# Optimization experiments

Measured on AMD Instinct MI355X. Metric: run time of the kernel, lower is better.

## Reference

```python
import jax, jax.numpy as jnp
import numpy as np

B, H, W, C = 4, 64, 64, 512
CR = C // 8  # reduced channel dim for query/key (conv_b, conv_c)


def setup_inputs() -> dict:
    key = jax.random.key(0)
    k1, k2, k3, k4, k5 = jax.random.split(key, 5)
    x = jax.random.normal(k1, (B, H, W, C), dtype=jnp.float32)
    # 1x1 conv kernels (no bias) == dense weights applied per pixel
    Wb = jax.random.normal(k2, (C, CR), dtype=jnp.float32) * (2.0 / C) ** 0.5
    Wc = jax.random.normal(k3, (C, CR), dtype=jnp.float32) * (2.0 / C) ** 0.5
    Wd = jax.random.normal(k4, (C, C), dtype=jnp.float32) * (2.0 / C) ** 0.5
    gamma = jax.random.normal(k5, (1,), dtype=jnp.float32)
    return {"x": x, "Wb": Wb, "Wc": Wc, "Wd": Wd, "gamma": gamma}


def reference(x, Wb, Wc, Wd, gamma):
    b, h, w, c = x.shape
    n = h * w
    xf = x.reshape(b, n, c)                       # [B,N,C] flatten spatial
    q = jnp.einsum('bnc,cd->bnd', xf, Wb)         # conv_b: [B,N,CR]
    k = jnp.einsum('bnc,cd->bnd', xf, Wc)         # conv_c: [B,N,CR]
    v = jnp.einsum('bnc,cd->bnd', xf, Wd)         # conv_d: [B,N,C]
    scores = jnp.einsum('bnd,bmd->bnm', q, k)     # [B,N,N] position affinities
    attn = jax.nn.softmax(scores, axis=-1)
    out = jnp.einsum('bnm,bmc->bnc', attn, v)     # [B,N,C]
    out = out.reshape(b, h, w, c)
    return gamma * out + x
```

## Files before the change

### kernel.cpp

```cpp
#include <hip/hip_runtime.h>


typedef __bf16 bf16_t;
typedef __bf16 bf16x8 __attribute__((ext_vector_type(8)));
typedef float f32x4 __attribute__((ext_vector_type(4)));
typedef unsigned long long u64;

#define NN 4096
#define CC 512
#define VSTRIDE 4160u
#define PSTRIDE 4160u
#define ESHIFT 90.0f

#define OFF_QH 0u
#define OFF_QL 1048576u
#define OFF_KH 2097152u
#define OFF_KL 3145728u
#define OFF_VT 4194304u
#define OFF_WBH 29491200u
#define OFF_WBL 29523968u
#define OFF_WCH 29556736u
#define OFF_WCL 29589504u
#define OFF_WD  29622272u
#define OFF_XHF 46137344u
#define OFF_XLF 54525952u
#define OFF_P   12713984u
#define PBATCH  17039360u

static __device__ __forceinline__ f32x4 mfma16(bf16x8 a, bf16x8 b, f32x4 c) {
    return __builtin_amdgcn_mfma_f32_16x16x32_bf16(a, b, c, 0, 0, 0);
}

static __device__ __forceinline__ void load_lds16(const bf16_t* g, bf16_t* l) {
    __builtin_amdgcn_global_load_lds(
        (const __attribute__((address_space(1))) unsigned int*)g,
        (__attribute__((address_space(3))) unsigned int*)l, 16, 0, 0);
}

__global__ __launch_bounds__(256) void prep_kernel(const float* __restrict__ Wb,
                                                   const float* __restrict__ Wc,
                                                   const float* __restrict__ Wd,
                                                   bf16_t* __restrict__ ws) {
    int j = blockIdx.x * 256 + threadIdx.x;
    if (j < 8192) {
        const float* W = (j < 4096) ? Wb : Wc;
        unsigned oh = (j < 4096) ? OFF_WBH : OFF_WCH;
        unsigned ol = (j < 4096) ? OFF_WBL : OFF_WCL;
        int jc = j & 4095;
        int nt = jc >> 10, ks = (jc >> 6) & 15, lane = jc & 63;
        int quad = lane >> 4, l16 = lane & 15;
        int col = nt * 16 + l16, k0 = ks * 32 + quad * 8;
        bf16x8 h, l;
#pragma unroll
        for (int i = 0; i < 8; ++i) {
            float v = W[(k0 + i) * 64 + col];
            bf16_t hv = (bf16_t)v;
            h[i] = hv;
            l[i] = (bf16_t)(v - (float)hv);
        }
        *(bf16x8*)(ws + oh + (size_t)jc * 8) = h;
        *(bf16x8*)(ws + ol + (size_t)jc * 8) = l;
    } else if (j < 40960) {
        int jc = j - 8192;
        int nT = jc >> 12, nt = (jc >> 10) & 3, ks = (jc >> 6) & 15, lane = jc & 63;
        int quad = lane >> 4, l16 = lane & 15;
        int col = nT * 64 + nt * 16 + l16, k0 = ks * 32 + quad * 8;
        bf16x8 h;
#pragma unroll
        for (int i = 0; i < 8; ++i)
            h[i] = (bf16_t)Wd[(k0 + i) * 512 + col];
        *(bf16x8*)(ws + OFF_WD + (size_t)jc * 8) = h;
    }
}

__global__ __launch_bounds__(256) void xprep_kernel(const float* __restrict__ x,
                                                    bf16_t* __restrict__ ws) {
    int mt = blockIdx.x;
    int tid = threadIdx.x;
    const float* xb = x + (size_t)mt * 32768;
#pragma unroll
    for (int it = 0; it < 16; ++it) {
        int c = it * 256 + tid;
        int row = c >> 6, col8 = c & 63;
        f32x4 a0 = *(const f32x4*)(xb + c * 8);
        f32x4 a1 = *(const f32x4*)(xb + c * 8 + 4);
        bf16x8 h, l;
#pragma unroll
        for (int jj = 0; jj < 4; ++jj) {
            bf16_t h0 = (bf16_t)a0[jj];
            bf16_t h1 = (bf16_t)a1[jj];
            h[jj] = h0;     l[jj] = (bf16_t)(a0[jj] - (float)h0);
            h[4 + jj] = h1; l[4 + jj] = (bf16_t)(a1[jj] - (float)h1);
        }
        int w = row >> 4, l16 = row & 15, ks = col8 >> 2, quad = col8 & 3;
        size_t dst = (size_t)mt * 32768 + w * 8192 + ks * 512 + (quad * 16 + l16) * 8;
        *(bf16x8*)(ws + OFF_XHF + dst) = h;
        *(bf16x8*)(ws + OFF_XLF + dst) = l;
    }
}

__global__ __launch_bounds__(256, 1) void qkv_kernel(bf16_t* __restrict__ ws) {
    int mt = blockIdx.x;
    int g  = blockIdx.y;
    int tid = threadIdx.x;
    int w = tid >> 6, lane = tid & 63, quad = lane >> 4, l16 = lane & 15;

    __shared__ __align__(16) bf16_t Vs[64][72];

    size_t xoff = (size_t)mt * 32768 + w * 8192 + lane * 8;

    if (g < 2) {
        bf16x8 xh[16], xl[16];
#pragma unroll
        for (int ks = 0; ks < 16; ++ks)
            xh[ks] = *(const bf16x8*)(ws + OFF_XHF + xoff + ks * 512);
#pragma unroll
        for (int ks = 0; ks < 16; ++ks)
            xl[ks] = *(const bf16x8*)(ws + OFF_XLF + xoff + ks * 512);

        const bf16_t* whf = ws + (g == 0 ? OFF_WBH : OFF_WCH) + lane * 8;
        const bf16_t* wlf = ws + (g == 0 ? OFF_WBL : OFF_WCL) + lane * 8;
        f32x4 acc[4];
#pragma unroll
        for (int nt = 0; nt < 4; ++nt) acc[nt] = (f32x4){0.f, 0.f, 0.f, 0.f};
#pragma unroll
        for (int ks = 0; ks < 16; ++ks) {
#pragma unroll
            for (int nt = 0; nt < 4; ++nt) {
                bf16x8 bh = *(const bf16x8*)(whf + (nt * 16 + ks) * 512);
                bf16x8 bl = *(const bf16x8*)(wlf + (nt * 16 + ks) * 512);
                acc[nt] = mfma16(xh[ks], bh, acc[nt]);
                acc[nt] = mfma16(xh[ks], bl, acc[nt]);
                acc[nt] = mfma16(xl[ks], bh, acc[nt]);
            }
        }
        unsigned base_h = (g == 0) ? OFF_QH : OFF_KH;
        unsigned base_l = (g == 0) ? OFF_QL : OFF_KL;
#pragma unroll
        for (int nt = 0; nt < 4; ++nt) {
            int gc = nt * 16 + l16;
#pragma unroll
            for (int r = 0; r < 4; ++r) {
                int gr = mt * 64 + w * 16 + quad * 4 + r;
                int b = gr >> 12, np = gr & 4095;
                float v = acc[nt][r];
                bf16_t h = (bf16_t)v;
                size_t o = ((size_t)(b * 4096 + np)) * 64 + gc;
                ws[base_h + o] = h;
                ws[base_l + o] = (bf16_t)(v - (float)h);
            }
        }
    } else {
        bf16x8 xh[16];
#pragma unroll
        for (int ks = 0; ks < 16; ++ks)
            xh[ks] = *(const bf16x8*)(ws + OFF_XHF + xoff + ks * 512);

        for (int t = 0; t < 2; ++t) {
            int nT = (g - 2) * 2 + t;
            const bf16_t* wdf = ws + OFF_WD + lane * 8;
            f32x4 acc[4];
#pragma unroll
            for (int nt = 0; nt < 4; ++nt) acc[nt] = (f32x4){0.f, 0.f, 0.f, 0.f};
#pragma unroll
            for (int ks = 0; ks < 16; ++ks) {
#pragma unroll
                for (int nt = 0; nt < 4; ++nt) {
                    bf16x8 bb = *(const bf16x8*)(wdf + (size_t)(((nT * 4 + nt) * 16 + ks)) * 512);
                    acc[nt] = mfma16(xh[ks], bb, acc[nt]);
                }
            }
#pragma unroll
            for (int nt = 0; nt < 4; ++nt) {
                bf16_t pk[4];
#pragma unroll
                for (int r = 0; r < 4; ++r) pk[r] = (bf16_t)acc[nt][r];
                *(u64*)&Vs[nt * 16 + l16][w * 16 + quad * 4] = *(u64*)pk;
            }
            __syncthreads();
            int gr0 = mt * 64;
            int bb = gr0 >> 12, np0 = gr0 & 4095;
            int ch = tid >> 2, seg = tid & 3;
            f32x4 d0 = *(const f32x4*)&Vs[ch][seg * 16];
            f32x4 d1 = *(const f32x4*)&Vs[ch][seg * 16 + 8];
            bf16_t* dst = ws + OFF_VT +
                ((size_t)bb * 512 + (size_t)(nT * 64 + ch)) * VSTRIDE + np0 + seg * 16;
            *(f32x4*)(dst) = d0;
            *(f32x4*)(dst + 8) = d1;
            __syncthreads();
        }
    }
}

__global__ __launch_bounds__(256, 2) void score_kernel(bf16_t* __restrict__ ws) {
    int idx = blockIdx.x;
    int mt = idx & 31;
    int nt = (idx >> 5) & 31;
    int b  = idx >> 10;
    int tid = threadIdx.x;
    int w = tid >> 6, lane = tid & 63, quad = lane >> 4, l16 = lane & 15;
    int wr = w >> 1, wc = w & 1;

    __shared__ __align__(16) bf16_t Ls[128][136];

    const bf16_t* Qh = ws + OFF_QH + (size_t)b * NN * 64;
    const bf16_t* Ql = ws + OFF_QL + (size_t)b * NN * 64;
    const bf16_t* Kh = ws + OFF_KH + (size_t)b * NN * 64;
    const bf16_t* Kl = ws + OFF_KL + (size_t)b * NN * 64;

    bf16x8 qh[4][2], ql[4][2];
#pragma unroll
    for (int rt = 0; rt < 4; ++rt) {
        size_t qo = (size_t)(nt * 128 + wr * 64 + rt * 16 + l16) * 64 + quad * 8;
        qh[rt][0] = *(const bf16x8*)(Qh + qo);
        qh[rt][1] = *(const bf16x8*)(Qh + qo + 32);
        ql[rt][0] = *(const bf16x8*)(Ql + qo);
        ql[rt][1] = *(const bf16x8*)(Ql + qo + 32);
    }

    f32x4 s[4][4];
#pragma unroll
    for (int ct = 0; ct < 4; ++ct) {
        size_t ko = (size_t)(mt * 128 + wc * 64 + ct * 16 + l16) * 64 + quad * 8;
        bf16x8 kh0 = *(const bf16x8*)(Kh + ko);
        bf16x8 kh1 = *(const bf16x8*)(Kh + ko + 32);
        bf16x8 kl0 = *(const bf16x8*)(Kl + ko);
        bf16x8 kl1 = *(const bf16x8*)(Kl + ko + 32);
#pragma unroll
        for (int rt = 0; rt < 4; ++rt) {
            f32x4 a = (f32x4){0.f, 0.f, 0.f, 0.f};
            a = mfma16(qh[rt][0], kh0, a);
            a = mfma16(qh[rt][1], kh1, a);
            a = mfma16(qh[rt][0], kl0, a);
            a = mfma16(qh[rt][1], kl1, a);
            a = mfma16(ql[rt][0], kh0, a);
            a = mfma16(ql[rt][1], kh1, a);
            s[rt][ct] = a;
        }
    }

#pragma unroll
    for (int rt = 0; rt < 4; ++rt)
#pragma unroll
        for (int ct = 0; ct < 4; ++ct)
#pragma unroll
            for (int r = 0; r < 4; ++r) {
                float p = __expf(s[rt][ct][r] - ESHIFT);
                Ls[wr * 64 + rt * 16 + quad * 4 + r][wc * 64 + ct * 16 + l16] = (bf16_t)p;
            }
    __syncthreads();

    bf16_t* P = ws + OFF_P + (size_t)b * PBATCH;
    int row0 = tid >> 4, chunk = tid & 15;
#pragma unroll
    for (int it = 0; it < 8; ++it) {
        int row = it * 16 + row0;
        f32x4 d = *(const f32x4*)&Ls[row][chunk * 8];
        *(f32x4*)(P + (size_t)(nt * 128 + row) * PSTRIDE + mt * 128 + chunk * 8) = d;
    }
}

__global__ __launch_bounds__(256, 2) void pv_kernel(const float* __restrict__ x,
                                                    const float* __restrict__ gamma_p,
                                                    const bf16_t* __restrict__ ws,
                                                    float* __restrict__ out) {
    int idx = blockIdx.x;
    int ct4 = idx & 3;
    int b   = (idx >> 2) & 3;
    int nt  = idx >> 4;
    int tid = threadIdx.x;
    int w = tid >> 6, lane = tid & 63, quad = lane >> 4, l16 = lane & 15;
    int wr = w >> 1, wc = w & 1;

    __shared__ __align__(16) bf16_t Pt[2][4096];
    __shared__ __align__(16) bf16_t Vt[2][4096];

    const bf16_t* P = ws + OFF_P + (size_t)b * PBATCH + (size_t)(nt * 128) * PSTRIDE;
    const bf16_t* V = ws + OFF_VT + (size_t)b * CC * VSTRIDE + (size_t)(ct4 * 128) * VSTRIDE;

    int sr = tid >> 2;
    int sc = (tid & 3) ^ ((sr >> 1) & 3);
    const bf16_t* gp = P + (size_t)sr * PSTRIDE + sc * 8;
    const bf16_t* gv = V + (size_t)sr * VSTRIDE + sc * 8;

    f32x4 o[4][4];
#pragma unroll
    for (int rt = 0; rt < 4; ++rt)
#pragma unroll
        for (int ct = 0; ct < 4; ++ct) o[rt][ct] = (f32x4){0.f, 0.f, 0.f, 0.f};
    f32x4 osum[4];
#pragma unroll
    for (int rt = 0; rt < 4; ++rt) osum[rt] = (f32x4){0.f, 0.f, 0.f, 0.f};

    bf16_t onev = (bf16_t)1.0f;
    bf16x8 vones = {onev, onev, onev, onev, onev, onev, onev, onev};

    auto stage = [&](int buf, int t) {
        int m0 = t * 32;
        load_lds16(gp + m0,                  &Pt[buf][tid * 8]);
        load_lds16(gp + 64u * PSTRIDE + m0,  &Pt[buf][2048 + tid * 8]);
        load_lds16(gv + m0,                  &Vt[buf][tid * 8]);
        load_lds16(gv + 64u * VSTRIDE + m0,  &Vt[buf][2048 + tid * 8]);
    };

    auto compute = [&](int buf) {
        bf16x8 pa[4], vb[4];
#pragma unroll
        for (int rt = 0; rt < 4; ++rt) {
            int R = wr * 64 + rt * 16 + l16;
            int mc = quad ^ ((R >> 1) & 3);
            pa[rt] = *(const bf16x8*)&Pt[buf][R * 32 + mc * 8];
        }
#pragma unroll
        for (int ct = 0; ct < 4; ++ct) {
            int Rv = wc * 64 + ct * 16 + l16;
            int mc = quad ^ ((Rv >> 1) & 3);
            vb[ct] = *(const bf16x8*)&Vt[buf][Rv * 32 + mc * 8];
        }
#pragma unroll
        for (int ct = 0; ct < 4; ++ct)
#pragma unroll
            for (int rt = 0; rt < 4; ++rt)
                o[rt][ct] = mfma16(pa[rt], vb[ct], o[rt][ct]);
        if (wc == 0) {
            osum[0] = mfma16(pa[0], vones, osum[0]);
            osum[1] = mfma16(pa[1], vones, osum[1]);
            osum[2] = mfma16(pa[2], vones, osum[2]);
            osum[3] = mfma16(pa[3], vones, osum[3]);
        }
    };

    stage(0, 0);
    __syncthreads();
    for (int t = 0; t < 127; ++t) {
        int cur = t & 1;
        stage(cur ^ 1, t + 1);
        compute(cur);
        __syncthreads();
    }
    compute(1);

    float* rsum_s = (float*)&Pt[0][0];
    if (wc == 0 && l16 == 0) {
#pragma unroll
        for (int rt = 0; rt < 4; ++rt)
#pragma unroll
            for (int r = 0; r < 4; ++r)
                rsum_s[wr * 64 + rt * 16 + quad * 4 + r] = osum[rt][r];
    }
    __syncthreads();

    float g = gamma_p[0];
#pragma unroll
    for (int rt = 0; rt < 4; ++rt) {
        f32x4 rs = *(const f32x4*)&rsum_s[wr * 64 + rt * 16 + quad * 4];
        f32x4 linv;
#pragma unroll
        for (int r = 0; r < 4; ++r) linv[r] = 1.0f / rs[r];
#pragma unroll
        for (int ct = 0; ct < 4; ++ct) {
#pragma unroll
            for (int r = 0; r < 4; ++r) {
                int n = nt * 128 + wr * 64 + rt * 16 + quad * 4 + r;
                int c = ct4 * 128 + wc * 64 + ct * 16 + l16;
                size_t off = ((size_t)(b * 4096 + n)) * 512 + c;
                out[off] = g * (o[rt][ct][r] * linv[r]) + x[off];
            }
        }
    }
}

extern "C" void kernel_launch(void* const* d_in, const int* in_sizes, int n_in,
                              void* d_out, int out_size, void* d_ws, size_t ws_size,
                              hipStream_t stream) {
    const float* x     = (const float*)d_in[0];
    const float* Wb    = (const float*)d_in[1];
    const float* Wc    = (const float*)d_in[2];
    const float* Wd    = (const float*)d_in[3];
    const float* gamma = (const float*)d_in[4];
    bf16_t* ws = (bf16_t*)d_ws;
    float* out = (float*)d_out;

    prep_kernel<<<160, 256, 0, stream>>>(Wb, Wc, Wd, ws);
    xprep_kernel<<<256, 256, 0, stream>>>(x, ws);
    qkv_kernel<<<dim3(256, 6), 256, 0, stream>>>(ws);
    score_kernel<<<4096, 256, 0, stream>>>(ws);
    pv_kernel<<<512, 256, 0, stream>>>(x, gamma, ws, out);
}
```

Baseline: 322.3 us.

## Triple-buffer PV kernel LDS staging with partial vmcnt waits

Changes the P·V kernel from double to triple buffering of the P and V tiles in shared memory, keeping two tile loads in flight ahead of compute. The single __syncthreads per step becomes a partial vmcnt wait plus a barrier, so the next tile's global-to-LDS loads can stay outstanding while the current tile computes. It raises LDS use from 32KB to 48KB per block, which may limit occupancy with launch bounds of 2 blocks per CU. It also depends on vmcnt counting being exact for the buffer loads.

```diff
diff --git a/kernel.cpp b/kernel.cpp
--- a/kernel.cpp
+++ b/kernel.cpp
@@ -272,8 +272,8 @@
     int w = tid >> 6, lane = tid & 63, quad = lane >> 4, l16 = lane & 15;
     int wr = w >> 1, wc = w & 1;
 
-    __shared__ __align__(16) bf16_t Pt[2][4096];
-    __shared__ __align__(16) bf16_t Vt[2][4096];
+    __shared__ __align__(16) bf16_t PtA[3 * 4096];
+    __shared__ __align__(16) bf16_t VtA[3 * 4096];
 
     const bf16_t* P = ws + OFF_P + (size_t)b * PBATCH + (size_t)(nt * 128) * PSTRIDE;
     const bf16_t* V = ws + OFF_VT + (size_t)b * CC * VSTRIDE + (size_t)(ct4 * 128) * VSTRIDE;
@@ -297,25 +297,29 @@
 
     auto stage = [&](int buf, int t) {
         int m0 = t * 32;
-        load_lds16(gp + m0,                  &Pt[buf][tid * 8]);
-        load_lds16(gp + 64u * PSTRIDE + m0,  &Pt[buf][2048 + tid * 8]);
-        load_lds16(gv + m0,                  &Vt[buf][tid * 8]);
-        load_lds16(gv + 64u * VSTRIDE + m0,  &Vt[buf][2048 + tid * 8]);
+        bf16_t* pd = PtA + buf * 4096;
+        bf16_t* vd = VtA + buf * 4096;
+        load_lds16(gp + m0,                  pd + tid * 8);
+        load_lds16(gp + 64u * PSTRIDE + m0,  pd + 2048 + tid * 8);
+        load_lds16(gv + m0,                  vd + tid * 8);
+        load_lds16(gv + 64u * VSTRIDE + m0,  vd + 2048 + tid * 8);
     };
 
     auto compute = [&](int buf) {
+        const bf16_t* pb = PtA + buf * 4096;
+        const bf16_t* vbuf = VtA + buf * 4096;
         bf16x8 pa[4], vb[4];
 #pragma unroll
         for (int rt = 0; rt < 4; ++rt) {
             int R = wr * 64 + rt * 16 + l16;
             int mc = quad ^ ((R >> 1) & 3);
-            pa[rt] = *(const bf16x8*)&Pt[buf][R * 32 + mc * 8];
+            pa[rt] = *(const bf16x8*)(pb + R * 32 + mc * 8);
         }
 #pragma unroll
         for (int ct = 0; ct < 4; ++ct) {
             int Rv = wc * 64 + ct * 16 + l16;
             int mc = quad ^ ((Rv >> 1) & 3);
-            vb[ct] = *(const bf16x8*)&Vt[buf][Rv * 32 + mc * 8];
+            vb[ct] = *(const bf16x8*)(vbuf + Rv * 32 + mc * 8);
         }
 #pragma unroll
         for (int ct = 0; ct < 4; ++ct)
@@ -330,17 +334,32 @@
         }
     };
 
+#define PV_SYNC(N)                                             \
+    asm volatile("s_waitcnt vmcnt(" #N ")" ::: "memory");      \
+    __builtin_amdgcn_s_barrier();                              \
+    __builtin_amdgcn_sched_barrier(0);
+
     stage(0, 0);
-    __syncthreads();
-    for (int t = 0; t < 127; ++t) {
-        int cur = t & 1;
-        stage(cur ^ 1, t + 1);
-        compute(cur);
-        __syncthreads();
-    }
+    stage(1, 1);
+
+    for (int tt = 0; tt < 126; tt += 3) {
+        PV_SYNC(4)
+        stage(2, tt + 2);
+        compute(0);
+        PV_SYNC(4)
+        stage(0, tt + 3);
+        compute(1);
+        PV_SYNC(4)
+        stage(1, tt + 4);
+        compute(2);
+    }
+    PV_SYNC(4)
+    compute(0);
+    PV_SYNC(0)
     compute(1);
-
-    float* rsum_s = (float*)&Pt[0][0];
+#undef PV_SYNC
+
+    float* rsum_s = (float*)&PtA[0];
     if (wc == 0 && l16 == 0) {
 #pragma unroll
         for (int rt = 0; rt < 4; ++rt)
```

Measured after the change: 319.4 us. No clear change (-0.9%).
